# Kernel optimization log

Measured on AMD Instinct MI355X. Metric: run time of the kernel, lower is better.

## Reference

```python
import jax, jax.numpy as jnp
import numpy as np

IGNORE_INDEX = -100
BETA = 0.1

def setup_inputs() -> dict:
    key = jax.random.key(0)
    k1, k2, k3, k4, k5, k6 = jax.random.split(key, 6)
    B, T, H, V = 4, 512, 2048, 32000
    x = jax.random.normal(k1, (B, T, H), dtype=jnp.float32)
    ref_x = jax.random.normal(k2, (B, T, H), dtype=jnp.float32)
    y = jax.random.randint(k3, (B, T), 0, V, dtype=jnp.int64)
    # mask a prefix of each sequence with ignore_index to exercise masking
    y = y.at[:, :10].set(IGNORE_INDEX)
    preference_labels = jax.random.randint(k4, (B,), 0, 2) == 1
    scale = 1.0 / np.sqrt(H)
    W = jax.random.normal(k5, (V, H), dtype=jnp.float32) * scale      # policy lm_head weight
    ref_W = jax.random.normal(k6, (V, H), dtype=jnp.float32) * scale  # reference lm_head weight
    return {"x": x, "ref_x": ref_x, "y": y, "preference_labels": preference_labels,
            "W": W, "ref_W": ref_W}


def _avg_target_logps(inp, w, y):
    # inp: (B, T, H), w: (V, H), y: (B, T) -> per-sequence average log-prob (B,)
    logits = jnp.einsum("bth,vh->btv", inp, w)
    logps = jax.nn.log_softmax(logits.astype(jnp.float32), axis=-1)
    mask = y != IGNORE_INDEX
    labels = jnp.where(mask, y, 0)
    tok_logps = jnp.take_along_axis(logps, labels[..., None], axis=-1)[..., 0]
    return (tok_logps * mask).sum(-1) / mask.sum(-1)


def reference(x, ref_x, y, preference_labels, W, ref_W):
    policy_logps = _avg_target_logps(x, W, y)                              # (B,)
    ref_logps = jax.lax.stop_gradient(_avg_target_logps(ref_x, ref_W, y))  # ref model under no_grad
    logratios = policy_logps - ref_logps
    multiplier = jnp.where(preference_labels, 1.0, -1.0)
    # KTO loss with KL term = 0 (policy_KL_logps / ref_KL_logps are None)
    losses = 1.0 - jax.nn.sigmoid(BETA * logratios * multiplier)
    return losses.sum() / y.shape[0]
```

## Files before the change

kernel.cpp:

```cpp
#include <hip/hip_runtime.h>
#include <math.h>

#define BATCH 4
#define TSEQ 512
#define MTOK 2048
#define HDIM 2048
#define VOCAB 32000
#define NCHUNK 500
#define IGNORE_INDEX (-100)
#define BETA 0.1f

typedef __attribute__((ext_vector_type(4))) float floatx4;
typedef __attribute__((ext_vector_type(8))) short short8;
typedef __attribute__((ext_vector_type(8))) unsigned short ushort8;

__device__ __forceinline__ unsigned short f2bf(float f) {
    unsigned int u = __float_as_uint(f);
    u += 0x7fffu + ((u >> 16) & 1u);
    return (unsigned short)(u >> 16);
}

__device__ __forceinline__ void async_copy16(const unsigned short* g, unsigned short* l) {
    __builtin_amdgcn_global_load_lds(
        (const __attribute__((address_space(1))) void*)g,
        (__attribute__((address_space(3))) void*)l, 16, 0, 0);
}

__global__ __launch_bounds__(256) void cvt_bf16_kernel(
        const float* __restrict__ src, unsigned short* __restrict__ dst) {
    size_t i = (size_t)blockIdx.x * 256 + threadIdx.x;
    const floatx4* s = (const floatx4*)src + i * 2;
    floatx4 a = s[0];
    floatx4 b = s[1];
    ushort8 o;
    o[0] = f2bf(a[0]); o[1] = f2bf(a[1]); o[2] = f2bf(a[2]); o[3] = f2bf(a[3]);
    o[4] = f2bf(b[0]); o[5] = f2bf(b[1]); o[6] = f2bf(b[2]); o[7] = f2bf(b[3]);
    *((ushort8*)dst + i) = o;
}

#define BK 64
__global__ __launch_bounds__(256, 2) void gemm_lse_kernel(
        const unsigned short* __restrict__ Xb,
        const unsigned short* __restrict__ Wb,
        const int* __restrict__ y,
        float* __restrict__ pmax,
        float* __restrict__ psum,
        float* __restrict__ tlog)
{
    __shared__ __align__(16) unsigned short sA[128 * BK];
    __shared__ __align__(16) unsigned short sB[128 * BK];

    const int tid  = threadIdx.x;
    const int m0   = blockIdx.x * 128;
    const int v0   = blockIdx.y * 128;
    const int w    = tid >> 6;
    const int lane = tid & 63;
    const int wm   = w & 1;
    const int wn   = w >> 1;
    const int c    = lane & 15;
    const int q    = lane >> 4;

    floatx4 acc[4][4] = {};

    const int e0 = tid * 8;

    for (int kt = 0; kt < HDIM / BK; ++kt) {
        const int k0 = kt * BK;
#pragma unroll
        for (int it = 0; it < 4; ++it) {
            int e   = it * 2048 + e0;
            int row = e >> 6;
            int p   = (e >> 3) & 7;
            int col = (p ^ (row & 7)) * 8;
            async_copy16(Xb + (size_t)(m0 + row) * HDIM + (k0 + col), &sA[e]);
            async_copy16(Wb + (size_t)(v0 + row) * HDIM + (k0 + col), &sB[e]);
        }
        __syncthreads();
#pragma unroll
        for (int kk = 0; kk < BK; kk += 32) {
            short8 af[4], bf[4];
            const int gq = (kk >> 3) + q;
            const int pq = gq ^ (c & 7);
#pragma unroll
            for (int i = 0; i < 4; ++i)
                af[i] = *(const short8*)&sA[(wm * 64 + i * 16 + c) * BK + pq * 8];
#pragma unroll
            for (int j = 0; j < 4; ++j)
                bf[j] = *(const short8*)&sB[(wn * 64 + j * 16 + c) * BK + pq * 8];
#pragma unroll
            for (int i = 0; i < 4; ++i)
#pragma unroll
                for (int j = 0; j < 4; ++j)
                    acc[i][j] = __builtin_amdgcn_mfma_f32_16x16x32_bf16(
                        af[i], bf[j], acc[i][j], 0, 0, 0);
        }
        __syncthreads();
    }

    const int chunk = blockIdx.y * 2 + wn;
#pragma unroll
    for (int i = 0; i < 4; ++i) {
        float mx[4], sm[4];
#pragma unroll
        for (int r = 0; r < 4; ++r) {
            float m4 = acc[i][0][r];
            m4 = fmaxf(m4, acc[i][1][r]);
            m4 = fmaxf(m4, acc[i][2][r]);
            m4 = fmaxf(m4, acc[i][3][r]);
            mx[r] = m4;
        }
#pragma unroll
        for (int d = 1; d < 16; d <<= 1)
#pragma unroll
            for (int r = 0; r < 4; ++r)
                mx[r] = fmaxf(mx[r], __shfl_xor(mx[r], d, 64));
#pragma unroll
        for (int r = 0; r < 4; ++r) {
            float s = 0.f;
#pragma unroll
            for (int j = 0; j < 4; ++j) s += expf(acc[i][j][r] - mx[r]);
            sm[r] = s;
        }
#pragma unroll
        for (int d = 1; d < 16; d <<= 1)
#pragma unroll
            for (int r = 0; r < 4; ++r)
                sm[r] += __shfl_xor(sm[r], d, 64);

        const int tokenBase = m0 + wm * 64 + i * 16 + q * 4;
        if (c == 0) {
#pragma unroll
            for (int r = 0; r < 4; ++r) {
                pmax[(size_t)(tokenBase + r) * NCHUNK + chunk] = mx[r];
                psum[(size_t)(tokenBase + r) * NCHUNK + chunk] = sm[r];
            }
        }
#pragma unroll
        for (int r = 0; r < 4; ++r) {
            int lab = y[tokenBase + r];
            int rel = lab - (v0 + wn * 64);
            if (rel >= 0 && rel < 64 && (rel & 15) == c) {
#pragma unroll
                for (int j = 0; j < 4; ++j)
                    if ((rel >> 4) == j)
                        tlog[tokenBase + r] = acc[i][j][r];
            }
        }
    }
}

__global__ __launch_bounds__(256) void finalize_kernel(
        const int* __restrict__ y,
        const float* __restrict__ pmax,
        const float* __restrict__ psum,
        const float* __restrict__ tlog,
        float* __restrict__ tokll, int slot) {
    const int wv    = threadIdx.x >> 6;
    const int lane  = threadIdx.x & 63;
    const int token = blockIdx.x * 4 + wv;

    const float* pm = &pmax[(size_t)token * NCHUNK];
    const float* ps = &psum[(size_t)token * NCHUNK];
    float m = -3.4e38f, s = 0.f;
    for (int c2 = lane; c2 < NCHUNK; c2 += 64) {
        float cm = pm[c2];
        float cs = ps[c2];
        if (cm > m) { s = s * expf(m - cm) + cs; m = cm; }
        else        { s += cs * expf(cm - m); }
    }
#pragma unroll
    for (int d = 1; d < 64; d <<= 1) {
        float om = __shfl_xor(m, d, 64);
        float os = __shfl_xor(s, d, 64);
        if (om > m) { s = s * expf(m - om) + os; m = om; }
        else        { s += os * expf(om - m); }
    }
    if (lane == 0) {
        int lab = y[token];
        float lse = m + logf(s);
        tokll[(size_t)slot * MTOK + token] =
            (lab == IGNORE_INDEX) ? 0.f : (tlog[token] - lse);
    }
}

__global__ __launch_bounds__(256) void seqreduce_kernel(
        const int* __restrict__ y,
        const float* __restrict__ tokll,
        float* __restrict__ seqavg) {
    const int slot = blockIdx.x >> 2;
    const int b    = blockIdx.x & 3;
    const int tid  = threadIdx.x;
    float lsum = 0.f, lcnt = 0.f;
    for (int t = tid; t < TSEQ; t += 256) {
        int token = b * TSEQ + t;
        lsum += tokll[(size_t)slot * MTOK + token];
        lcnt += (y[token] != IGNORE_INDEX) ? 1.f : 0.f;
    }
    __shared__ float rs[256];
    __shared__ float rc[256];
    rs[tid] = lsum; rc[tid] = lcnt;
    __syncthreads();
    for (int s2 = 128; s2 > 0; s2 >>= 1) {
        if (tid < s2) { rs[tid] += rs[tid + s2]; rc[tid] += rc[tid + s2]; }
        __syncthreads();
    }
    if (tid == 0) seqavg[slot * BATCH + b] = rs[0] / rc[0];
}

__global__ void kto_loss_kernel(const float* __restrict__ seqavg,
                                const int* __restrict__ pref,
                                float* __restrict__ out) {
    if (threadIdx.x == 0 && blockIdx.x == 0) {
        float acc = 0.f;
        for (int b = 0; b < BATCH; ++b) {
            float lr   = seqavg[b] - seqavg[BATCH + b];
            float mult = pref[b] ? 1.f : -1.f;
            float z    = BETA * lr * mult;
            float sig  = 1.f / (1.f + expf(-z));
            acc += 1.f - sig;
        }
        out[0] = acc * (1.f / (float)BATCH);
    }
}

extern "C" void kernel_launch(void* const* d_in, const int* in_sizes, int n_in,
                              void* d_out, int out_size, void* d_ws, size_t ws_size,
                              hipStream_t stream) {
    const float* x      = (const float*)d_in[0];
    const float* ref_x  = (const float*)d_in[1];
    const int*   y      = (const int*)d_in[2];
    const int*   pref   = (const int*)d_in[3];
    const float* W      = (const float*)d_in[4];
    const float* ref_W  = (const float*)d_in[5];
    float* out = (float*)d_out;
    char*  ws  = (char*)d_ws;

    const size_t WBF_OFF  = 0;
    const size_t XBF_OFF  = WBF_OFF + (size_t)VOCAB * HDIM * 2;
    const size_t PMAX_OFF = XBF_OFF + (size_t)MTOK * HDIM * 2;
    const size_t PSUM_OFF = PMAX_OFF + (size_t)MTOK * NCHUNK * 4;
    const size_t TLOG_OFF = PSUM_OFF + (size_t)MTOK * NCHUNK * 4;
    const size_t TOKL_OFF = TLOG_OFF + (size_t)MTOK * 4;
    const size_t SEQ_OFF  = TOKL_OFF + (size_t)2 * MTOK * 4;

    unsigned short* wbf  = (unsigned short*)(ws + WBF_OFF);
    unsigned short* xbf  = (unsigned short*)(ws + XBF_OFF);
    float* pmax   = (float*)(ws + PMAX_OFF);
    float* psum   = (float*)(ws + PSUM_OFF);
    float* tlog   = (float*)(ws + TLOG_OFF);
    float* tokll  = (float*)(ws + TOKL_OFF);
    float* seqavg = (float*)(ws + SEQ_OFF);

    for (int model = 0; model < 2; ++model) {
        const float* xin = model ? ref_x : x;
        const float* win = model ? ref_W : W;
        cvt_bf16_kernel<<<VOCAB * HDIM / 2048, 256, 0, stream>>>(win, wbf);
        cvt_bf16_kernel<<<MTOK * HDIM / 2048, 256, 0, stream>>>(xin, xbf);
        gemm_lse_kernel<<<dim3(MTOK / 128, VOCAB / 128), 256, 0, stream>>>(
            xbf, wbf, y, pmax, psum, tlog);
        finalize_kernel<<<MTOK / 4, 256, 0, stream>>>(y, pmax, psum, tlog, tokll, model);
    }
    seqreduce_kernel<<<8, 256, 0, stream>>>(y, tokll, seqavg);
    kto_loss_kernel<<<1, 64, 0, stream>>>(seqavg, pref, out);
}
```

Measured before the change: 1.108 ms.

## Batch both models into single conversion, GEMM, finalize and tail launches

```diff
diff --git a/kernel.cpp b/kernel.cpp
--- a/kernel.cpp
+++ b/kernel.cpp
@@ -10,6 +10,9 @@
 #define IGNORE_INDEX (-100)
 #define BETA 0.1f
 
+#define WBLK (VOCAB * HDIM / 2048)
+#define XBLK (MTOK * HDIM / 2048)
+
 typedef __attribute__((ext_vector_type(4))) float floatx4;
 typedef __attribute__((ext_vector_type(8))) short short8;
 typedef __attribute__((ext_vector_type(8))) unsigned short ushort8;
@@ -26,9 +29,9 @@
         (__attribute__((address_space(3))) void*)l, 16, 0, 0);
 }
 
-__global__ __launch_bounds__(256) void cvt_bf16_kernel(
-        const float* __restrict__ src, unsigned short* __restrict__ dst) {
-    size_t i = (size_t)blockIdx.x * 256 + threadIdx.x;
+__device__ __forceinline__ void cvt_block(const float* __restrict__ src,
+                                          unsigned short* __restrict__ dst,
+                                          size_t i) {
     const floatx4* s = (const floatx4*)src + i * 2;
     floatx4 a = s[0];
     floatx4 b = s[1];
@@ -38,17 +41,45 @@
     *((ushort8*)dst + i) = o;
 }
 
+__global__ __launch_bounds__(256) void cvt_bf16_kernel(
+        const float* __restrict__ src, unsigned short* __restrict__ dst) {
+    cvt_block(src, dst, (size_t)blockIdx.x * 256 + threadIdx.x);
+}
+
+__global__ __launch_bounds__(256) void cvt_all_kernel(
+        const float* __restrict__ s0, const float* __restrict__ s1,
+        const float* __restrict__ s2, const float* __restrict__ s3,
+        unsigned short* __restrict__ d0, unsigned short* __restrict__ d1,
+        unsigned short* __restrict__ d2, unsigned short* __restrict__ d3) {
+    int b = blockIdx.x;
+    const float* src;
+    unsigned short* dst;
+    int rel;
+    if (b < WBLK)              { src = s0; dst = d0; rel = b; }
+    else if (b < 2 * WBLK)     { src = s1; dst = d1; rel = b - WBLK; }
+    else if (b < 2*WBLK + XBLK){ src = s2; dst = d2; rel = b - 2*WBLK; }
+    else                       { src = s3; dst = d3; rel = b - 2*WBLK - XBLK; }
+    cvt_block(src, dst, (size_t)rel * 256 + threadIdx.x);
+}
+
 #define BK 64
 __global__ __launch_bounds__(256, 2) void gemm_lse_kernel(
-        const unsigned short* __restrict__ Xb,
-        const unsigned short* __restrict__ Wb,
+        const unsigned short* __restrict__ Xb0,
+        const unsigned short* __restrict__ Xb1,
+        const unsigned short* __restrict__ Wb0,
+        const unsigned short* __restrict__ Wb1,
         const int* __restrict__ y,
         float* __restrict__ pmax,
         float* __restrict__ psum,
-        float* __restrict__ tlog)
+        float* __restrict__ tlog,
+        int slot_base)
 {
     __shared__ __align__(16) unsigned short sA[128 * BK];
     __shared__ __align__(16) unsigned short sB[128 * BK];
+
+    const int slot = slot_base + blockIdx.z;
+    const unsigned short* __restrict__ Xb = slot ? Xb1 : Xb0;
+    const unsigned short* __restrict__ Wb = slot ? Wb1 : Wb0;
 
     const int tid  = threadIdx.x;
     const int m0   = blockIdx.x * 128;
@@ -131,8 +162,8 @@
         if (c == 0) {
 #pragma unroll
             for (int r = 0; r < 4; ++r) {
-                pmax[(size_t)(tokenBase + r) * NCHUNK + chunk] = mx[r];
-                psum[(size_t)(tokenBase + r) * NCHUNK + chunk] = sm[r];
+                pmax[(size_t)(slot * MTOK + tokenBase + r) * NCHUNK + chunk] = mx[r];
+                psum[(size_t)(slot * MTOK + tokenBase + r) * NCHUNK + chunk] = sm[r];
             }
         }
 #pragma unroll
@@ -143,7 +174,7 @@
 #pragma unroll
                 for (int j = 0; j < 4; ++j)
                     if ((rel >> 4) == j)
-                        tlog[tokenBase + r] = acc[i][j][r];
+                        tlog[(size_t)slot * MTOK + tokenBase + r] = acc[i][j][r];
             }
         }
     }
@@ -154,13 +185,14 @@
         const float* __restrict__ pmax,
         const float* __restrict__ psum,
         const float* __restrict__ tlog,
-        float* __restrict__ tokll, int slot) {
+        float* __restrict__ tokll, int slot_base) {
     const int wv    = threadIdx.x >> 6;
     const int lane  = threadIdx.x & 63;
     const int token = blockIdx.x * 4 + wv;
-
-    const float* pm = &pmax[(size_t)token * NCHUNK];
-    const float* ps = &psum[(size_t)token * NCHUNK];
+    const int slot  = slot_base + blockIdx.y;
+
+    const float* pm = &pmax[(size_t)(slot * MTOK + token) * NCHUNK];
+    const float* ps = &psum[(size_t)(slot * MTOK + token) * NCHUNK];
     float m = -3.4e38f, s = 0.f;
     for (int c2 = lane; c2 < NCHUNK; c2 += 64) {
         float cm = pm[c2];
@@ -179,38 +211,38 @@
         int lab = y[token];
         float lse = m + logf(s);
         tokll[(size_t)slot * MTOK + token] =
-            (lab == IGNORE_INDEX) ? 0.f : (tlog[token] - lse);
-    }
-}
-
-__global__ __launch_bounds__(256) void seqreduce_kernel(
+            (lab == IGNORE_INDEX) ? 0.f : (tlog[(size_t)slot * MTOK + token] - lse);
+    }
+}
+
+__global__ __launch_bounds__(256) void tail_kernel(
         const int* __restrict__ y,
         const float* __restrict__ tokll,
-        float* __restrict__ seqavg) {
-    const int slot = blockIdx.x >> 2;
-    const int b    = blockIdx.x & 3;
-    const int tid  = threadIdx.x;
-    float lsum = 0.f, lcnt = 0.f;
-    for (int t = tid; t < TSEQ; t += 256) {
-        int token = b * TSEQ + t;
-        lsum += tokll[(size_t)slot * MTOK + token];
-        lcnt += (y[token] != IGNORE_INDEX) ? 1.f : 0.f;
-    }
+        const int* __restrict__ pref,
+        float* __restrict__ out) {
     __shared__ float rs[256];
     __shared__ float rc[256];
-    rs[tid] = lsum; rc[tid] = lcnt;
-    __syncthreads();
-    for (int s2 = 128; s2 > 0; s2 >>= 1) {
-        if (tid < s2) { rs[tid] += rs[tid + s2]; rc[tid] += rc[tid + s2]; }
+    __shared__ float seqavg[8];
+    const int tid = threadIdx.x;
+    for (int sb = 0; sb < 8; ++sb) {
+        const int slot = sb >> 2;
+        const int b    = sb & 3;
+        float lsum = 0.f, lcnt = 0.f;
+        for (int t = tid; t < TSEQ; t += 256) {
+            int token = b * TSEQ + t;
+            lsum += tokll[(size_t)slot * MTOK + token];
+            lcnt += (y[token] != IGNORE_INDEX) ? 1.f : 0.f;
+        }
+        rs[tid] = lsum; rc[tid] = lcnt;
         __syncthreads();
-    }
-    if (tid == 0) seqavg[slot * BATCH + b] = rs[0] / rc[0];
-}
-
-__global__ void kto_loss_kernel(const float* __restrict__ seqavg,
-                                const int* __restrict__ pref,
-                                float* __restrict__ out) {
-    if (threadIdx.x == 0 && blockIdx.x == 0) {
+        for (int s2 = 128; s2 > 0; s2 >>= 1) {
+            if (tid < s2) { rs[tid] += rs[tid + s2]; rc[tid] += rc[tid + s2]; }
+            __syncthreads();
+        }
+        if (tid == 0) seqavg[sb] = rs[0] / rc[0];
+        __syncthreads();
+    }
+    if (tid == 0) {
         float acc = 0.f;
         for (int b = 0; b < BATCH; ++b) {
             float lr   = seqavg[b] - seqavg[BATCH + b];
@@ -235,31 +267,47 @@
     float* out = (float*)d_out;
     char*  ws  = (char*)d_ws;
 
-    const size_t WBF_OFF  = 0;
-    const size_t XBF_OFF  = WBF_OFF + (size_t)VOCAB * HDIM * 2;
-    const size_t PMAX_OFF = XBF_OFF + (size_t)MTOK * HDIM * 2;
-    const size_t PSUM_OFF = PMAX_OFF + (size_t)MTOK * NCHUNK * 4;
-    const size_t TLOG_OFF = PSUM_OFF + (size_t)MTOK * NCHUNK * 4;
-    const size_t TOKL_OFF = TLOG_OFF + (size_t)MTOK * 4;
-    const size_t SEQ_OFF  = TOKL_OFF + (size_t)2 * MTOK * 4;
-
-    unsigned short* wbf  = (unsigned short*)(ws + WBF_OFF);
-    unsigned short* xbf  = (unsigned short*)(ws + XBF_OFF);
-    float* pmax   = (float*)(ws + PMAX_OFF);
-    float* psum   = (float*)(ws + PSUM_OFF);
-    float* tlog   = (float*)(ws + TLOG_OFF);
-    float* tokll  = (float*)(ws + TOKL_OFF);
-    float* seqavg = (float*)(ws + SEQ_OFF);
-
-    for (int model = 0; model < 2; ++model) {
-        const float* xin = model ? ref_x : x;
-        const float* win = model ? ref_W : W;
-        cvt_bf16_kernel<<<VOCAB * HDIM / 2048, 256, 0, stream>>>(win, wbf);
-        cvt_bf16_kernel<<<MTOK * HDIM / 2048, 256, 0, stream>>>(xin, xbf);
-        gemm_lse_kernel<<<dim3(MTOK / 128, VOCAB / 128), 256, 0, stream>>>(
-            xbf, wbf, y, pmax, psum, tlog);
-        finalize_kernel<<<MTOK / 4, 256, 0, stream>>>(y, pmax, psum, tlog, tokll, model);
-    }
-    seqreduce_kernel<<<8, 256, 0, stream>>>(y, tokll, seqavg);
-    kto_loss_kernel<<<1, 64, 0, stream>>>(seqavg, pref, out);
-}
+    const size_t WSZ = (size_t)VOCAB * HDIM * 2;
+    const size_t XSZ = (size_t)MTOK * HDIM * 2;
+    const size_t PSZ = (size_t)2 * MTOK * NCHUNK * 4;
+
+    const size_t need_dual = 2*WSZ + 2*XSZ + 2*PSZ + (size_t)4*MTOK*4 + 4096;
+
+    if (ws_size >= need_dual) {
+        unsigned short* wbf0 = (unsigned short*)(ws);
+        unsigned short* wbf1 = (unsigned short*)(ws + WSZ);
+        unsigned short* xbf0 = (unsigned short*)(ws + 2*WSZ);
+        unsigned short* xbf1 = (unsigned short*)(ws + 2*WSZ + XSZ);
+        float* pmax  = (float*)(ws + 2*WSZ + 2*XSZ);
+        float* psum  = (float*)(ws + 2*WSZ + 2*XSZ + PSZ);
+        float* tlog  = (float*)(ws + 2*WSZ + 2*XSZ + 2*PSZ);
+        float* tokll = (float*)(ws + 2*WSZ + 2*XSZ + 2*PSZ + (size_t)2*MTOK*4);
+
+        cvt_all_kernel<<<2*WBLK + 2*XBLK, 256, 0, stream>>>(
+            W, ref_W, x, ref_x, wbf0, wbf1, xbf0, xbf1);
+        gemm_lse_kernel<<<dim3(MTOK/128, VOCAB/128, 2), 256, 0, stream>>>(
+            xbf0, xbf1, wbf0, wbf1, y, pmax, psum, tlog, 0);
+        finalize_kernel<<<dim3(MTOK/4, 2), 256, 0, stream>>>(
+            y, pmax, psum, tlog, tokll, 0);
+        tail_kernel<<<1, 256, 0, stream>>>(y, tokll, pref, out);
+    } else {
+        unsigned short* wbf = (unsigned short*)(ws);
+        unsigned short* xbf = (unsigned short*)(ws + WSZ);
+        float* pmax  = (float*)(ws + WSZ + XSZ);
+        float* psum  = (float*)(ws + WSZ + XSZ + PSZ);
+        float* tlog  = (float*)(ws + WSZ + XSZ + 2*PSZ);
+        float* tokll = (float*)(ws + WSZ + XSZ + 2*PSZ + (size_t)2*MTOK*4);
+
+        for (int model = 0; model < 2; ++model) {
+            const float* xin = model ? ref_x : x;
+            const float* win = model ? ref_W : W;
+            cvt_bf16_kernel<<<WBLK, 256, 0, stream>>>(win, wbf);
+            cvt_bf16_kernel<<<XBLK, 256, 0, stream>>>(xin, xbf);
+            gemm_lse_kernel<<<dim3(MTOK/128, VOCAB/128, 1), 256, 0, stream>>>(
+                xbf, xbf, wbf, wbf, y, pmax, psum, tlog, model);
+            finalize_kernel<<<dim3(MTOK/4, 1), 256, 0, stream>>>(
+                y, pmax, psum, tlog, tokll, model);
+        }
+        tail_kernel<<<1, 256, 0, stream>>>(y, tokll, pref, out);
+    }
+}
```

Measured after the change: 1.104 ms. No clear change (-0.4%).
